# Kernel optimization log

Measured on AMD Instinct MI355X. Metric: run time of the kernel, lower is better.

Reference implementation:

```python
import jax, jax.numpy as jnp
import numpy as np

DIM = 64  # per-head dim used for the sqrt scale


def setup_inputs() -> dict:
    key = jax.random.key(0)
    kq, kk, kv, ke, kf = jax.random.split(key, 5)
    B, N, d, k = 32, 4096, 64, 256
    Q = jax.random.normal(kq, (B, N, d), dtype=jnp.float32)
    K = jax.random.normal(kk, (B, N, d), dtype=jnp.float32)
    V = jax.random.normal(kv, (B, N, d), dtype=jnp.float32)
    E = jax.random.normal(ke, (N, k), dtype=jnp.float32) * (1.0 / np.sqrt(N))
    F = jax.random.normal(kf, (N, k), dtype=jnp.float32) * (1.0 / np.sqrt(N))
    return {"Q": Q, "K": K, "V": V, "E": E, "F": F}


def reference(Q, K, V, E, F):
    # Linformer head: K^T E -> [B,d,k]; Q (K^T E) / sqrt(d) -> [B,N,k]
    K_proj = jnp.einsum('bnd,nk->bdk', K, E)          # low-rank key projection
    scores = jnp.einsum('bnd,bdk->bnk', Q, K_proj) / jnp.sqrt(jnp.float32(DIM))
    P_bar = jax.nn.softmax(scores, axis=2)            # [B,N,k]
    # (V^T F)^T -> [B,k,d]
    V_proj = jnp.einsum('bnd,nk->bkd', V, F)
    return jnp.einsum('bnk,bkd->bnd', P_bar, V_proj)  # [B,N,d]
```

## Files before the change

kernel.cpp:

```cpp
#include <hip/hip_runtime.h>
#include <hip/hip_bf16.h>

#define BB 32
#define NN 4096
#define DDIM 64
#define NCH 8

typedef __attribute__((ext_vector_type(8)))  short bf16x8;
typedef __attribute__((ext_vector_type(16))) float f32x16;
typedef __attribute__((ext_vector_type(4)))  float f32x4;

static __device__ inline unsigned short f2bf(float x) {
  union { float f; unsigned u; } v; v.f = x;
  unsigned r = (v.u + 0x7FFFu + ((v.u >> 16) & 1u)) >> 16;
  return (unsigned short)r;
}

static __device__ inline unsigned pk(float a, float b) {
  union { __hip_bfloat162 h; unsigned u; } c;
  c.h = __float22bfloat162_rn(float2{a, b});
  return c.u;
}

__global__ __launch_bounds__(256) void prep_frag(
    const float* __restrict__ Eg, const float* __restrict__ Fg,
    const float* __restrict__ Kg, const float* __restrict__ Vg,
    unsigned short* __restrict__ Ebt, unsigned short* __restrict__ Fbt,
    unsigned short* __restrict__ Kbt, unsigned short* __restrict__ Vbt)
{
  const int blk = blockIdx.x, t = threadIdx.x;
  float v[8];
  if (blk < 1024) {
    const int which = blk >> 9;
    const int nbg = blk & 511;
    const float* src = (which ? Fg : Eg) + (long)(nbg * 8) * 256 + t;
    unsigned short* dst = (which ? Fbt : Ebt) + ((long)nbg * 256 + t) * 8;
#pragma unroll
    for (int j = 0; j < 8; ++j) v[j] = src[j * 256];
    union { unsigned u[4]; bf16x8 x; } r;
    r.u[0] = pk(v[0], v[1]); r.u[1] = pk(v[2], v[3]);
    r.u[2] = pk(v[4], v[5]); r.u[3] = pk(v[6], v[7]);
    *(bf16x8*)dst = r.x;
  } else {
    const int kb = blk - 1024;
    const int which = kb >> 12;
    const int kb2 = kb & 4095;
    const int b = kb2 >> 7, nb = kb2 & 127;
    const int g = t >> 6, d = t & 63;
    const int nbg = nb * 4 + g;
    const float* src = (which ? Vg : Kg) + ((long)b * NN + nbg * 8) * 64 + d;
    unsigned short* dst = (which ? Vbt : Kbt)
                        + (long)b * 262144 + ((long)nbg * 64 + d) * 8;
#pragma unroll
    for (int j = 0; j < 8; ++j) v[j] = src[j * 64];
    union { unsigned u[4]; bf16x8 x; } r;
    r.u[0] = pk(v[0], v[1]); r.u[1] = pk(v[2], v[3]);
    r.u[2] = pk(v[4], v[5]); r.u[3] = pk(v[6], v[7]);
    *(bf16x8*)dst = r.x;
  }
}

template <int MAT>
static __device__ inline void proj_core5(
    const unsigned short* __restrict__ Bigt,
    const unsigned short* __restrict__ Smlt,
    float* __restrict__ Cg, int w, int h, int lr, int chunk)
{
  f32x16 acc[2][2];
#pragma unroll
  for (int i = 0; i < 2; ++i)
#pragma unroll
    for (int j = 0; j < 2; ++j)
#pragma unroll
      for (int q = 0; q < 16; ++q) acc[i][j][q] = 0.f;

  const int colB = w * 64 + lr;
  const unsigned short* pB0 = Bigt + (((long)chunk * 16 * 4 + h) * 256 + colB) * 8;
  const unsigned short* pB1 = pB0 + 2 * 256 * 8;
  const unsigned short* pS0 = Smlt + (((long)chunk * 16 * 4 + h) * 64 + lr) * 8;
  const unsigned short* pS1 = pS0 + 2 * 64 * 8;

#pragma unroll 4
  for (int tt = 0; tt < 16; ++tt) {
    const long ob = (long)tt * (1024 * 8);
    const long os = (long)tt * (256 * 8);
    bf16x8 B0a = *(const bf16x8*)(pB0 + ob);
    bf16x8 B0b = *(const bf16x8*)(pB0 + ob + 32 * 8);
    bf16x8 B1a = *(const bf16x8*)(pB1 + ob);
    bf16x8 B1b = *(const bf16x8*)(pB1 + ob + 32 * 8);
    bf16x8 S0a = *(const bf16x8*)(pS0 + os);
    bf16x8 S0b = *(const bf16x8*)(pS0 + os + 32 * 8);
    bf16x8 S1a = *(const bf16x8*)(pS1 + os);
    bf16x8 S1b = *(const bf16x8*)(pS1 + os + 32 * 8);
    if (MAT == 0) {
      acc[0][0] = __builtin_amdgcn_mfma_f32_32x32x16_bf16(B0a, S0a, acc[0][0], 0, 0, 0);
      acc[0][1] = __builtin_amdgcn_mfma_f32_32x32x16_bf16(B0a, S0b, acc[0][1], 0, 0, 0);
      acc[1][0] = __builtin_amdgcn_mfma_f32_32x32x16_bf16(B0b, S0a, acc[1][0], 0, 0, 0);
      acc[1][1] = __builtin_amdgcn_mfma_f32_32x32x16_bf16(B0b, S0b, acc[1][1], 0, 0, 0);
      acc[0][0] = __builtin_amdgcn_mfma_f32_32x32x16_bf16(B1a, S1a, acc[0][0], 0, 0, 0);
      acc[0][1] = __builtin_amdgcn_mfma_f32_32x32x16_bf16(B1a, S1b, acc[0][1], 0, 0, 0);
      acc[1][0] = __builtin_amdgcn_mfma_f32_32x32x16_bf16(B1b, S1a, acc[1][0], 0, 0, 0);
      acc[1][1] = __builtin_amdgcn_mfma_f32_32x32x16_bf16(B1b, S1b, acc[1][1], 0, 0, 0);
    } else {
      acc[0][0] = __builtin_amdgcn_mfma_f32_32x32x16_bf16(S0a, B0a, acc[0][0], 0, 0, 0);
      acc[0][1] = __builtin_amdgcn_mfma_f32_32x32x16_bf16(S0a, B0b, acc[0][1], 0, 0, 0);
      acc[1][0] = __builtin_amdgcn_mfma_f32_32x32x16_bf16(S0b, B0a, acc[1][0], 0, 0, 0);
      acc[1][1] = __builtin_amdgcn_mfma_f32_32x32x16_bf16(S0b, B0b, acc[1][1], 0, 0, 0);
      acc[0][0] = __builtin_amdgcn_mfma_f32_32x32x16_bf16(S1a, B1a, acc[0][0], 0, 0, 0);
      acc[0][1] = __builtin_amdgcn_mfma_f32_32x32x16_bf16(S1a, B1b, acc[0][1], 0, 0, 0);
      acc[1][0] = __builtin_amdgcn_mfma_f32_32x32x16_bf16(S1b, B1a, acc[1][0], 0, 0, 0);
      acc[1][1] = __builtin_amdgcn_mfma_f32_32x32x16_bf16(S1b, B1b, acc[1][1], 0, 0, 0);
    }
  }

  const int mAdd = (MAT == 0) ? w * 64 : 0;
  const int nAdd = (MAT == 0) ? 0 : w * 64;
  const int OS   = (MAT == 0) ? 64 : 256;
#pragma unroll
  for (int mt = 0; mt < 2; ++mt)
#pragma unroll
    for (int nt = 0; nt < 2; ++nt)
#pragma unroll
      for (int i = 0; i < 16; ++i) {
        int ro  = (i & 3) + 8 * (i >> 2) + 4 * h;
        int row = mAdd + mt * 32 + ro;
        int col = nAdd + nt * 32 + lr;
        Cg[row * OS + col] = acc[mt][nt][i];
      }
}

__global__ __launch_bounds__(256, 2) void proj_gemm(
    const unsigned short* __restrict__ Ebt, const unsigned short* __restrict__ Fbt,
    const unsigned short* __restrict__ Kbt, const unsigned short* __restrict__ Vbt,
    float* __restrict__ KpP, float* __restrict__ VpP)
{
  const int blk = blockIdx.x;
  const int chunk = blk % NCH;
  const int mat = (blk / NCH) & 1, b = blk / (2 * NCH);
  const int t = threadIdx.x, w = t >> 6, l = t & 63, h = l >> 5, lr = l & 31;
  const long PSTR = (long)BB * 16384;

  if (mat == 0) {
    proj_core5<0>(Ebt, Kbt + (long)b * 262144,
                  KpP + (long)chunk * PSTR + b * 16384, w, h, lr, chunk);
  } else {
    proj_core5<1>(Fbt, Vbt + (long)b * 262144,
                  VpP + (long)chunk * PSTR + b * 16384, w, h, lr, chunk);
  }
}

__global__ __launch_bounds__(256) void reduce_cvt(
    const float* __restrict__ KpP, const float* __restrict__ VpP,
    unsigned short* __restrict__ Kpb, unsigned short* __restrict__ Vpb)
{
  const int blk = blockIdx.x;
  const float* src = (blk < 256) ? KpP : VpP;
  unsigned short* dst = (blk < 256) ? Kpb : Vpb;
  const long i = (long)(blk & 255) * 2048 + threadIdx.x * 8;
  float a[8];
#pragma unroll
  for (int j = 0; j < 8; ++j) a[j] = 0.f;
#pragma unroll
  for (int cch = 0; cch < NCH; ++cch) {
    const float4 p0 = *(const float4*)(src + (long)cch * (BB * 16384) + i);
    const float4 p1 = *(const float4*)(src + (long)cch * (BB * 16384) + i + 4);
    a[0] += p0.x; a[1] += p0.y; a[2] += p0.z; a[3] += p0.w;
    a[4] += p1.x; a[5] += p1.y; a[6] += p1.z; a[7] += p1.w;
  }
  unsigned short o[8];
#pragma unroll
  for (int j = 0; j < 8; ++j) o[j] = f2bf(a[j]);
  *(bf16x8*)(dst + i) = *(const bf16x8*)&o[0];
}

__global__ __launch_bounds__(256, 2) void attn2_kernel(
    const float* __restrict__ Qg, const unsigned short* __restrict__ Kpb,
    const unsigned short* __restrict__ Vpb, float* __restrict__ Og)
{
  extern __shared__ char smem[];

  const int blk = blockIdx.x;
  const int b = blk >> 4, rg = blk & 15;
  const int t = threadIdx.x, w = t >> 6, l = t & 63;
  const int h = l >> 5, lr = l & 31;
  const int rbase = rg * 256 + w * 64;

  bf16x8 Bq[2][4];
#pragma unroll
  for (int rt = 0; rt < 2; ++rt)
#pragma unroll
    for (int kk = 0; kk < 4; ++kk) {
      const float* qp = Qg + ((long)b * NN + rbase + rt * 32 + lr) * 64 + kk * 16 + h * 8;
      float4 x = *(const float4*)qp;
      float4 y = *(const float4*)(qp + 4);
      union { unsigned u[4]; bf16x8 v; } r;
      r.u[0] = pk(x.x, x.y); r.u[1] = pk(x.z, x.w);
      r.u[2] = pk(y.x, y.y); r.u[3] = pk(y.z, y.w);
      Bq[rt][kk] = r.v;
    }

  {
    const uint4* gk = (const uint4*)(Kpb + (long)b * 16384);
    const uint4* gv = (const uint4*)(Vpb + (long)b * 16384);
#pragma unroll
    for (int i = 0; i < 8; ++i) {
      int u = i * 256 + t;
      uint4 x = gk[u];
      int kbyte = (u * 16) ^ (((u >> 3) & 7) << 4);
      *(uint4*)(smem + kbyte) = x;
      uint4 y = gv[u];
      int vbyte = (u * 16) ^ (((u >> 5) & 7) << 4);
      *(uint4*)(smem + 32768 + vbyte) = y;
    }
  }
  __syncthreads();

  f32x16 o[2][2];
#pragma unroll
  for (int rt = 0; rt < 2; ++rt)
#pragma unroll
    for (int dt = 0; dt < 2; ++dt)
#pragma unroll
      for (int q = 0; q < 16; ++q) o[rt][dt][q] = 0.f;
  float rowpart[2] = {0.f, 0.f};

  union UV { uint4 u; bf16x8 v; };
  const int swz = (lr & 7) << 4;

#pragma unroll
  for (int kt = 0; kt < 8; ++kt) {
    bf16x8 Ak[4];
#pragma unroll
    for (int kk = 0; kk < 4; ++kk) {
      int byte = (kt * 32 + lr) * 128 + kk * 32 + h * 16;
      Ak[kk] = *(const bf16x8*)(smem + (byte ^ swz));
    }
    bf16x8 Av[2][2];
#pragma unroll
    for (int dt = 0; dt < 2; ++dt)
#pragma unroll
      for (int kc = 0; kc < 2; ++kc) {
        int byte = (dt * 32 + lr) * 512 + (kt * 2 + kc) * 32 + h * 16;
        Av[dt][kc] = *(const bf16x8*)(smem + 32768 + (byte ^ swz));
      }

#pragma unroll
    for (int rt = 0; rt < 2; ++rt) {
      f32x16 s;
#pragma unroll
      for (int q = 0; q < 16; ++q) s[q] = 0.f;
#pragma unroll
      for (int kk = 0; kk < 4; ++kk)
        s = __builtin_amdgcn_mfma_f32_32x32x16_bf16(Ak[kk], Bq[rt][kk], s, 0, 0, 0);

      float p[16];
#pragma unroll
      for (int q = 0; q < 16; ++q) p[q] = exp2f(s[q] * 0.1803368801f);
      rowpart[rt] += (((p[0] + p[1]) + (p[2] + p[3])) + ((p[4] + p[5]) + (p[6] + p[7])))
                   + (((p[8] + p[9]) + (p[10] + p[11])) + ((p[12] + p[13]) + (p[14] + p[15])));

      unsigned wv[8];
#pragma unroll
      for (int m = 0; m < 8; ++m) wv[m] = pk(p[2 * m], p[2 * m + 1]);
      unsigned r02 = __shfl_xor(h ? wv[0] : wv[2], 32);
      unsigned r13 = __shfl_xor(h ? wv[1] : wv[3], 32);
      unsigned r46 = __shfl_xor(h ? wv[4] : wv[6], 32);
      unsigned r57 = __shfl_xor(h ? wv[5] : wv[7], 32);
      UV c0, c1;
      if (h == 0) {
        c0.u = uint4{wv[0], wv[1], r02, r13};
        c1.u = uint4{wv[4], wv[5], r46, r57};
      } else {
        c0.u = uint4{r02, r13, wv[2], wv[3]};
        c1.u = uint4{r46, r57, wv[6], wv[7]};
      }
      o[rt][0] = __builtin_amdgcn_mfma_f32_32x32x16_bf16(Av[0][0], c0.v, o[rt][0], 0, 0, 0);
      o[rt][0] = __builtin_amdgcn_mfma_f32_32x32x16_bf16(Av[0][1], c1.v, o[rt][0], 0, 0, 0);
      o[rt][1] = __builtin_amdgcn_mfma_f32_32x32x16_bf16(Av[1][0], c0.v, o[rt][1], 0, 0, 0);
      o[rt][1] = __builtin_amdgcn_mfma_f32_32x32x16_bf16(Av[1][1], c1.v, o[rt][1], 0, 0, 0);
    }
  }

  __syncthreads();
  float* O_lds = (float*)smem;

#pragma unroll
  for (int rt = 0; rt < 2; ++rt) {
    float rowsum = rowpart[rt] + __shfl_xor(rowpart[rt], 32);
    float inv = __builtin_amdgcn_rcpf(rowsum);
    const int r = w * 64 + rt * 32 + lr;
#pragma unroll
    for (int dt = 0; dt < 2; ++dt)
#pragma unroll
      for (int qg = 0; qg < 4; ++qg) {
        f32x4 vq;
        vq[0] = o[rt][dt][qg * 4 + 0] * inv;
        vq[1] = o[rt][dt][qg * 4 + 1] * inv;
        vq[2] = o[rt][dt][qg * 4 + 2] * inv;
        vq[3] = o[rt][dt][qg * 4 + 3] * inv;
        int cd = dt * 8 + 2 * qg + h;
        int cp = cd ^ (r & 15);
        *(f32x4*)&O_lds[r * 64 + cp * 4] = vq;
      }
  }
  __syncthreads();

  const long obase = ((long)b * NN + rg * 256) * 64;
#pragma unroll
  for (int i = 0; i < 16; ++i) {
    int ci = i * 256 + t;
    int rr = ci >> 4, cc = ci & 15, cp = cc ^ (rr & 15);
    *(float4*)(Og + obase + rr * 64 + cc * 4) = *(const float4*)&O_lds[rr * 64 + cp * 4];
  }
}

extern "C" void kernel_launch(void* const* d_in, const int* in_sizes, int n_in,
                              void* d_out, int out_size, void* d_ws, size_t ws_size,
                              hipStream_t stream) {
  const float* Q = (const float*)d_in[0];
  const float* K = (const float*)d_in[1];
  const float* V = (const float*)d_in[2];
  const float* E = (const float*)d_in[3];
  const float* F = (const float*)d_in[4];
  float* out = (float*)d_out;

  char* ws = (char*)d_ws;
  float*          KpP = (float*)(ws);
  float*          VpP = (float*)(ws + (16l << 20));
  unsigned short* Kpb = (unsigned short*)(ws + (32l << 20));
  unsigned short* Vpb = (unsigned short*)(ws + (33l << 20));
  unsigned short* Ebt = (unsigned short*)(ws + (34l << 20));
  unsigned short* Fbt = (unsigned short*)(ws + (36l << 20));
  unsigned short* Kbt = (unsigned short*)(ws + (38l << 20));
  unsigned short* Vbt = (unsigned short*)(ws + (54l << 20));

  hipFuncSetAttribute((const void*)attn2_kernel,
                      hipFuncAttributeMaxDynamicSharedMemorySize, 65536);

  prep_frag<<<dim3(9216), dim3(256), 0, stream>>>(E, F, K, V, Ebt, Fbt, Kbt, Vbt);

  proj_gemm<<<dim3(512), dim3(256), 0, stream>>>(Ebt, Fbt, Kbt, Vbt, KpP, VpP);

  reduce_cvt<<<dim3(512), dim3(256), 0, stream>>>(KpP, VpP, Kpb, Vpb);

  attn2_kernel<<<dim3(512), dim3(256), 65536, stream>>>(Q, Kpb, Vpb, out);
}
```

Before: 193.1 us.

## Replace split-K partial buffers and reduce kernel with atomic accumulation; retile attention

The projection GEMM now accumulates its split-N chunks directly into a zeroed fp32 buffer with relaxed atomic adds, so the separate reduce/convert kernel and the 8x partial buffers go away. The attention kernel reads the fp32 projections directly, converting K_proj to bf16 into LDS and loading V_proj fragments from global per iteration. It also halves rows per block (1024 blocks, 32 KB LDS, occupancy hint 4). This removes one launch and the partial-sum traffic but adds a memset and atomic contention, and has every block re-read V_proj from global/L2.

```diff
diff --git a/kernel.cpp b/kernel.cpp
--- a/kernel.cpp
+++ b/kernel.cpp
@@ -9,12 +9,6 @@
 typedef __attribute__((ext_vector_type(8)))  short bf16x8;
 typedef __attribute__((ext_vector_type(16))) float f32x16;
 typedef __attribute__((ext_vector_type(4)))  float f32x4;
-
-static __device__ inline unsigned short f2bf(float x) {
-  union { float f; unsigned u; } v; v.f = x;
-  unsigned r = (v.u + 0x7FFFu + ((v.u >> 16) & 1u)) >> 16;
-  return (unsigned short)r;
-}
 
 static __device__ inline unsigned pk(float a, float b) {
   union { __hip_bfloat162 h; unsigned u; } c;
@@ -125,7 +119,8 @@
         int ro  = (i & 3) + 8 * (i >> 2) + 4 * h;
         int row = mAdd + mt * 32 + ro;
         int col = nAdd + nt * 32 + lr;
-        Cg[row * OS + col] = acc[mt][nt][i];
+        __hip_atomic_fetch_add(&Cg[row * OS + col], acc[mt][nt][i],
+                               __ATOMIC_RELAXED, __HIP_MEMORY_SCOPE_AGENT);
       }
 }
 
@@ -138,166 +133,141 @@
   const int chunk = blk % NCH;
   const int mat = (blk / NCH) & 1, b = blk / (2 * NCH);
   const int t = threadIdx.x, w = t >> 6, l = t & 63, h = l >> 5, lr = l & 31;
-  const long PSTR = (long)BB * 16384;
 
   if (mat == 0) {
     proj_core5<0>(Ebt, Kbt + (long)b * 262144,
-                  KpP + (long)chunk * PSTR + b * 16384, w, h, lr, chunk);
+                  KpP + (long)b * 16384, w, h, lr, chunk);
   } else {
     proj_core5<1>(Fbt, Vbt + (long)b * 262144,
-                  VpP + (long)chunk * PSTR + b * 16384, w, h, lr, chunk);
-  }
-}
-
-__global__ __launch_bounds__(256) void reduce_cvt(
-    const float* __restrict__ KpP, const float* __restrict__ VpP,
-    unsigned short* __restrict__ Kpb, unsigned short* __restrict__ Vpb)
+                  VpP + (long)b * 16384, w, h, lr, chunk);
+  }
+}
+
+__global__ __launch_bounds__(256, 4) void attn2_kernel(
+    const float* __restrict__ Qg, const float* __restrict__ KpP,
+    const float* __restrict__ VpP, float* __restrict__ Og)
 {
+  __shared__ char smem[32768];
+
   const int blk = blockIdx.x;
-  const float* src = (blk < 256) ? KpP : VpP;
-  unsigned short* dst = (blk < 256) ? Kpb : Vpb;
-  const long i = (long)(blk & 255) * 2048 + threadIdx.x * 8;
-  float a[8];
-#pragma unroll
-  for (int j = 0; j < 8; ++j) a[j] = 0.f;
-#pragma unroll
-  for (int cch = 0; cch < NCH; ++cch) {
-    const float4 p0 = *(const float4*)(src + (long)cch * (BB * 16384) + i);
-    const float4 p1 = *(const float4*)(src + (long)cch * (BB * 16384) + i + 4);
-    a[0] += p0.x; a[1] += p0.y; a[2] += p0.z; a[3] += p0.w;
-    a[4] += p1.x; a[5] += p1.y; a[6] += p1.z; a[7] += p1.w;
-  }
-  unsigned short o[8];
-#pragma unroll
-  for (int j = 0; j < 8; ++j) o[j] = f2bf(a[j]);
-  *(bf16x8*)(dst + i) = *(const bf16x8*)&o[0];
-}
-
-__global__ __launch_bounds__(256, 2) void attn2_kernel(
-    const float* __restrict__ Qg, const unsigned short* __restrict__ Kpb,
-    const unsigned short* __restrict__ Vpb, float* __restrict__ Og)
-{
-  extern __shared__ char smem[];
-
-  const int blk = blockIdx.x;
-  const int b = blk >> 4, rg = blk & 15;
+  const int b = blk >> 5, rg = blk & 31;
   const int t = threadIdx.x, w = t >> 6, l = t & 63;
   const int h = l >> 5, lr = l & 31;
-  const int rbase = rg * 256 + w * 64;
-
-  bf16x8 Bq[2][4];
-#pragma unroll
-  for (int rt = 0; rt < 2; ++rt)
+  const int row0 = rg * 128 + w * 32;
+
+  const float* Kp = KpP + (long)b * 16384;
+  const float* Vp = VpP + (long)b * 16384;
+
+  bf16x8 Bq[4];
+#pragma unroll
+  for (int kk = 0; kk < 4; ++kk) {
+    const float* qp = Qg + ((long)b * NN + row0 + lr) * 64 + kk * 16 + h * 8;
+    float4 x = *(const float4*)qp;
+    float4 y = *(const float4*)(qp + 4);
+    union { unsigned u[4]; bf16x8 v; } r;
+    r.u[0] = pk(x.x, x.y); r.u[1] = pk(x.z, x.w);
+    r.u[2] = pk(y.x, y.y); r.u[3] = pk(y.z, y.w);
+    Bq[kk] = r.v;
+  }
+
+  {
+    const float4* gk = (const float4*)Kp;
+#pragma unroll
+    for (int j = 0; j < 16; ++j) {
+      int u = j * 256 + t;
+      float4 x = gk[u];
+      unsigned lo = pk(x.x, x.y), hi = pk(x.z, x.w);
+      int e = u * 4;
+      int row = e >> 6, col = e & 63;
+      int byte = (row * 128 + col * 2) ^ ((row & 7) << 4);
+      *(uint2*)(smem + byte) = uint2{lo, hi};
+    }
+  }
+  __syncthreads();
+
+  f32x16 o[2];
+#pragma unroll
+  for (int dt = 0; dt < 2; ++dt)
+#pragma unroll
+    for (int q = 0; q < 16; ++q) o[dt][q] = 0.f;
+  float rowpart = 0.f;
+
+  union UV { uint4 u; bf16x8 v; };
+
+#pragma unroll
+  for (int kt = 0; kt < 8; ++kt) {
+    bf16x8 Av[2][2];
+#pragma unroll
+    for (int dt = 0; dt < 2; ++dt)
+#pragma unroll
+      for (int kc = 0; kc < 2; ++kc) {
+        const float* vp = Vp + (long)(dt * 32 + lr) * 256 + (kt * 2 + kc) * 16 + h * 8;
+        float4 x = *(const float4*)vp;
+        float4 y = *(const float4*)(vp + 4);
+        union { unsigned u[4]; bf16x8 v; } r;
+        r.u[0] = pk(x.x, x.y); r.u[1] = pk(x.z, x.w);
+        r.u[2] = pk(y.x, y.y); r.u[3] = pk(y.z, y.w);
+        Av[dt][kc] = r.v;
+      }
+
+    bf16x8 Ak[4];
 #pragma unroll
     for (int kk = 0; kk < 4; ++kk) {
-      const float* qp = Qg + ((long)b * NN + rbase + rt * 32 + lr) * 64 + kk * 16 + h * 8;
-      float4 x = *(const float4*)qp;
-      float4 y = *(const float4*)(qp + 4);
-      union { unsigned u[4]; bf16x8 v; } r;
-      r.u[0] = pk(x.x, x.y); r.u[1] = pk(x.z, x.w);
-      r.u[2] = pk(y.x, y.y); r.u[3] = pk(y.z, y.w);
-      Bq[rt][kk] = r.v;
+      int row = kt * 32 + lr;
+      int byte = (row * 128 + kk * 32 + h * 16) ^ ((row & 7) << 4);
+      Ak[kk] = *(const bf16x8*)(smem + byte);
     }
 
-  {
-    const uint4* gk = (const uint4*)(Kpb + (long)b * 16384);
-    const uint4* gv = (const uint4*)(Vpb + (long)b * 16384);
-#pragma unroll
-    for (int i = 0; i < 8; ++i) {
-      int u = i * 256 + t;
-      uint4 x = gk[u];
-      int kbyte = (u * 16) ^ (((u >> 3) & 7) << 4);
-      *(uint4*)(smem + kbyte) = x;
-      uint4 y = gv[u];
-      int vbyte = (u * 16) ^ (((u >> 5) & 7) << 4);
-      *(uint4*)(smem + 32768 + vbyte) = y;
+    f32x16 s;
+#pragma unroll
+    for (int q = 0; q < 16; ++q) s[q] = 0.f;
+#pragma unroll
+    for (int kk = 0; kk < 4; ++kk)
+      s = __builtin_amdgcn_mfma_f32_32x32x16_bf16(Ak[kk], Bq[kk], s, 0, 0, 0);
+
+    float p[16];
+#pragma unroll
+    for (int q = 0; q < 16; ++q) p[q] = exp2f(s[q] * 0.1803368801f);
+    rowpart += (((p[0] + p[1]) + (p[2] + p[3])) + ((p[4] + p[5]) + (p[6] + p[7])))
+             + (((p[8] + p[9]) + (p[10] + p[11])) + ((p[12] + p[13]) + (p[14] + p[15])));
+
+    unsigned wv[8];
+#pragma unroll
+    for (int m = 0; m < 8; ++m) wv[m] = pk(p[2 * m], p[2 * m + 1]);
+    unsigned r02 = __shfl_xor(h ? wv[0] : wv[2], 32);
+    unsigned r13 = __shfl_xor(h ? wv[1] : wv[3], 32);
+    unsigned r46 = __shfl_xor(h ? wv[4] : wv[6], 32);
+    unsigned r57 = __shfl_xor(h ? wv[5] : wv[7], 32);
+    UV c0, c1;
+    if (h == 0) {
+      c0.u = uint4{wv[0], wv[1], r02, r13};
+      c1.u = uint4{wv[4], wv[5], r46, r57};
+    } else {
+      c0.u = uint4{r02, r13, wv[2], wv[3]};
+      c1.u = uint4{r46, r57, wv[6], wv[7]};
     }
-  }
-  __syncthreads();
-
-  f32x16 o[2][2];
-#pragma unroll
-  for (int rt = 0; rt < 2; ++rt)
-#pragma unroll
-    for (int dt = 0; dt < 2; ++dt)
-#pragma unroll
-      for (int q = 0; q < 16; ++q) o[rt][dt][q] = 0.f;
-  float rowpart[2] = {0.f, 0.f};
-
-  union UV { uint4 u; bf16x8 v; };
-  const int swz = (lr & 7) << 4;
-
-#pragma unroll
-  for (int kt = 0; kt < 8; ++kt) {
-    bf16x8 Ak[4];
-#pragma unroll
-    for (int kk = 0; kk < 4; ++kk) {
-      int byte = (kt * 32 + lr) * 128 + kk * 32 + h * 16;
-      Ak[kk] = *(const bf16x8*)(smem + (byte ^ swz));
-    }
-    bf16x8 Av[2][2];
-#pragma unroll
-    for (int dt = 0; dt < 2; ++dt)
-#pragma unroll
-      for (int kc = 0; kc < 2; ++kc) {
-        int byte = (dt * 32 + lr) * 512 + (kt * 2 + kc) * 32 + h * 16;
-        Av[dt][kc] = *(const bf16x8*)(smem + 32768 + (byte ^ swz));
-      }
-
-#pragma unroll
-    for (int rt = 0; rt < 2; ++rt) {
-      f32x16 s;
-#pragma unroll
-      for (int q = 0; q < 16; ++q) s[q] = 0.f;
-#pragma unroll
-      for (int kk = 0; kk < 4; ++kk)
-        s = __builtin_amdgcn_mfma_f32_32x32x16_bf16(Ak[kk], Bq[rt][kk], s, 0, 0, 0);
-
-      float p[16];
-#pragma unroll
-      for (int q = 0; q < 16; ++q) p[q] = exp2f(s[q] * 0.1803368801f);
-      rowpart[rt] += (((p[0] + p[1]) + (p[2] + p[3])) + ((p[4] + p[5]) + (p[6] + p[7])))
-                   + (((p[8] + p[9]) + (p[10] + p[11])) + ((p[12] + p[13]) + (p[14] + p[15])));
-
-      unsigned wv[8];
-#pragma unroll
-      for (int m = 0; m < 8; ++m) wv[m] = pk(p[2 * m], p[2 * m + 1]);
-      unsigned r02 = __shfl_xor(h ? wv[0] : wv[2], 32);
-      unsigned r13 = __shfl_xor(h ? wv[1] : wv[3], 32);
-      unsigned r46 = __shfl_xor(h ? wv[4] : wv[6], 32);
-      unsigned r57 = __shfl_xor(h ? wv[5] : wv[7], 32);
-      UV c0, c1;
-      if (h == 0) {
-        c0.u = uint4{wv[0], wv[1], r02, r13};
-        c1.u = uint4{wv[4], wv[5], r46, r57};
-      } else {
-        c0.u = uint4{r02, r13, wv[2], wv[3]};
-        c1.u = uint4{r46, r57, wv[6], wv[7]};
-      }
-      o[rt][0] = __builtin_amdgcn_mfma_f32_32x32x16_bf16(Av[0][0], c0.v, o[rt][0], 0, 0, 0);
-      o[rt][0] = __builtin_amdgcn_mfma_f32_32x32x16_bf16(Av[0][1], c1.v, o[rt][0], 0, 0, 0);
-      o[rt][1] = __builtin_amdgcn_mfma_f32_32x32x16_bf16(Av[1][0], c0.v, o[rt][1], 0, 0, 0);
-      o[rt][1] = __builtin_amdgcn_mfma_f32_32x32x16_bf16(Av[1][1], c1.v, o[rt][1], 0, 0, 0);
-    }
+    o[0] = __builtin_amdgcn_mfma_f32_32x32x16_bf16(Av[0][0], c0.v, o[0], 0, 0, 0);
+    o[0] = __builtin_amdgcn_mfma_f32_32x32x16_bf16(Av[0][1], c1.v, o[0], 0, 0, 0);
+    o[1] = __builtin_amdgcn_mfma_f32_32x32x16_bf16(Av[1][0], c0.v, o[1], 0, 0, 0);
+    o[1] = __builtin_amdgcn_mfma_f32_32x32x16_bf16(Av[1][1], c1.v, o[1], 0, 0, 0);
   }
 
   __syncthreads();
   float* O_lds = (float*)smem;
 
-#pragma unroll
-  for (int rt = 0; rt < 2; ++rt) {
-    float rowsum = rowpart[rt] + __shfl_xor(rowpart[rt], 32);
+  {
+    float rowsum = rowpart + __shfl_xor(rowpart, 32);
     float inv = __builtin_amdgcn_rcpf(rowsum);
-    const int r = w * 64 + rt * 32 + lr;
+    const int r = w * 32 + lr;
 #pragma unroll
     for (int dt = 0; dt < 2; ++dt)
 #pragma unroll
       for (int qg = 0; qg < 4; ++qg) {
         f32x4 vq;
-        vq[0] = o[rt][dt][qg * 4 + 0] * inv;
-        vq[1] = o[rt][dt][qg * 4 + 1] * inv;
-        vq[2] = o[rt][dt][qg * 4 + 2] * inv;
-        vq[3] = o[rt][dt][qg * 4 + 3] * inv;
+        vq[0] = o[dt][qg * 4 + 0] * inv;
+        vq[1] = o[dt][qg * 4 + 1] * inv;
+        vq[2] = o[dt][qg * 4 + 2] * inv;
+        vq[3] = o[dt][qg * 4 + 3] * inv;
         int cd = dt * 8 + 2 * qg + h;
         int cp = cd ^ (r & 15);
         *(f32x4*)&O_lds[r * 64 + cp * 4] = vq;
@@ -305,9 +275,9 @@
   }
   __syncthreads();
 
-  const long obase = ((long)b * NN + rg * 256) * 64;
-#pragma unroll
-  for (int i = 0; i < 16; ++i) {
+  const long obase = ((long)b * NN + rg * 128) * 64;
+#pragma unroll
+  for (int i = 0; i < 8; ++i) {
     int ci = i * 256 + t;
     int rr = ci >> 4, cc = ci & 15, cp = cc ^ (rr & 15);
     *(float4*)(Og + obase + rr * 64 + cc * 4) = *(const float4*)&O_lds[rr * 64 + cp * 4];
@@ -326,22 +296,17 @@
 
   char* ws = (char*)d_ws;
   float*          KpP = (float*)(ws);
-  float*          VpP = (float*)(ws + (16l << 20));
-  unsigned short* Kpb = (unsigned short*)(ws + (32l << 20));
-  unsigned short* Vpb = (unsigned short*)(ws + (33l << 20));
-  unsigned short* Ebt = (unsigned short*)(ws + (34l << 20));
-  unsigned short* Fbt = (unsigned short*)(ws + (36l << 20));
-  unsigned short* Kbt = (unsigned short*)(ws + (38l << 20));
-  unsigned short* Vbt = (unsigned short*)(ws + (54l << 20));
-
-  hipFuncSetAttribute((const void*)attn2_kernel,
-                      hipFuncAttributeMaxDynamicSharedMemorySize, 65536);
+  float*          VpP = (float*)(ws + (2l << 20));
+  unsigned short* Ebt = (unsigned short*)(ws + (4l << 20));
+  unsigned short* Fbt = (unsigned short*)(ws + (6l << 20));
+  unsigned short* Kbt = (unsigned short*)(ws + (8l << 20));
+  unsigned short* Vbt = (unsigned short*)(ws + (24l << 20));
+
+  hipMemsetAsync(ws, 0, 4l << 20, stream);
 
   prep_frag<<<dim3(9216), dim3(256), 0, stream>>>(E, F, K, V, Ebt, Fbt, Kbt, Vbt);
 
   proj_gemm<<<dim3(512), dim3(256), 0, stream>>>(Ebt, Fbt, Kbt, Vbt, KpP, VpP);
 
-  reduce_cvt<<<dim3(512), dim3(256), 0, stream>>>(KpP, VpP, Kpb, Vpb);
-
-  attn2_kernel<<<dim3(512), dim3(256), 65536, stream>>>(Q, Kpb, Vpb, out);
-}
+  attn2_kernel<<<dim3(1024), dim3(256), 0, stream>>>(Q, KpP, VpP, out);
+}
```

After: 250.4 us. 1.3x slower.
